# Kernel optimization log

Hardware: AMD Instinct MI355X
Metric: run time of the kernel (lower is better)

## Reference

```python
import jax, jax.numpy as jnp
import numpy as np

B, N, D = 4, 2048, 1024
H, A, Lv = 8, 128, 128   # heads, attention_dim (qk), linear_dim (v)
NUM_BLOCKS = 4
QKV_W = (2 * Lv + 2 * A) * H  # 4096
NEG = -1e9


def setup_inputs() -> dict:
    key = jax.random.key(0)
    ks = jax.random.split(key, 10)
    past_lengths = jax.random.randint(ks[0], (B,), 0, N)
    past_ids = jax.random.randint(ks[1], (B, N), 0, 10000)
    past_embeddings = jax.random.normal(ks[2], (B, N, D), dtype=jnp.float32)
    # per-block parameters, stacked on leading block axis (xavier-ish scale)
    qkv_w = jax.random.normal(ks[3], (NUM_BLOCKS, D, QKV_W), dtype=jnp.float32) * (1.0 / np.sqrt(D))
    qkv_b = jnp.zeros((NUM_BLOCKS, QKV_W), dtype=jnp.float32)
    out_w = jax.random.normal(ks[4], (NUM_BLOCKS, Lv * H, D), dtype=jnp.float32) * (1.0 / np.sqrt(Lv * H))
    out_b = jnp.zeros((NUM_BLOCKS, D), dtype=jnp.float32)
    ln_g = jnp.ones((NUM_BLOCKS, D), dtype=jnp.float32)
    ln_b = jnp.zeros((NUM_BLOCKS, D), dtype=jnp.float32)
    return {"past_lengths": past_lengths, "past_ids": past_ids,
            "past_embeddings": past_embeddings, "qkv_w": qkv_w, "qkv_b": qkv_b,
            "out_w": out_w, "out_b": out_b, "ln_g": ln_g, "ln_b": ln_b}


def _layer_norm(x, g, b, eps=1e-5):
    mu = jnp.mean(x, axis=-1, keepdims=True)
    var = jnp.mean(jnp.square(x - mu), axis=-1, keepdims=True)
    return (x - mu) * jax.lax.rsqrt(var + eps) * g + b


def _block(x, mask, qw, qb, ow, ob, g, b):
    xn = _layer_norm(x, g, b)
    qkv = (xn @ qw + qb).reshape(B, N, H, 2 * Lv + 2 * A)
    q = qkv[..., :A]              # [B,N,H,A]
    k = qkv[..., A:2 * A]         # [B,N,H,A]
    v = qkv[..., 2 * A:2 * A + Lv]  # [B,N,H,Lv]
    scores = jnp.einsum('bnha,bmha->bhnm', q, k) / np.sqrt(A)
    # original: masked_fill(-inf) -> silu -> /N -> softmax; we mask after the
    # silu transform with a large-negative logit so masked weights are ~0
    logits = jnp.where(mask[:, None, :, :], jax.nn.silu(scores) / N, NEG)
    w = jax.nn.softmax(logits, axis=-1)
    attn = jnp.einsum('bhnm,bmhl->bnhl', w, v).reshape(B, N, H * Lv)
    return x + attn @ ow + ob


def reference(past_lengths, past_ids, past_embeddings, qkv_w, qkv_b, out_w, out_b, ln_g, ln_b):
    valid = past_ids != 0                                   # [B,N]
    causal = jnp.triu(jnp.ones((N, N), dtype=bool), k=1)     # faithful to buffer (triu, diag=1)
    mask = causal[None] & valid[:, None, :] & valid[:, :, None]  # [B,N,N]
    x = past_embeddings
    for i in range(NUM_BLOCKS):
        x = _block(x, mask, qkv_w[i], qkv_b[i], out_w[i], out_b[i], ln_g[i], ln_b[i])
    return x
```

## Files before the change

### kernel.cpp

```cpp
#include <hip/hip_runtime.h>

typedef __bf16 bf16_t;
typedef __bf16 bf16x8 __attribute__((ext_vector_type(8)));
typedef __bf16 bf16x4 __attribute__((ext_vector_type(4)));
typedef float f32x4 __attribute__((ext_vector_type(4)));

#define B_ 4
#define N_ 2048
#define D_ 1024
#define H_ 8
#define NB_ 4
#define M_ (B_*N_)
#define QN_ 3072
#define QKN_ 2048

__device__ __forceinline__ void async_copy16(const void* gsrc, void* ldst) {
    __builtin_amdgcn_global_load_lds(
        (const __attribute__((address_space(1))) void*)gsrc,
        (__attribute__((address_space(3))) void*)ldst, 16, 0, 0);
}

static constexpr size_t WT_OFF  = 0;
static constexpr size_t WT_SZ   = (size_t)NB_*QN_*D_*2;
static constexpr size_t OWT_OFF = WT_OFF + WT_SZ;
static constexpr size_t OWT_SZ  = (size_t)NB_*D_*D_*2;
static constexpr size_t XN_OFF  = OWT_OFF + OWT_SZ;
static constexpr size_t XN_SZ   = (size_t)M_*D_*2;
static constexpr size_t QK_OFF  = XN_OFF + XN_SZ;
static constexpr size_t QK_SZ   = (size_t)M_*QKN_*2;
static constexpr size_t VT_OFF  = QK_OFF + QK_SZ;
static constexpr size_t VT_SZ   = (size_t)32*128*N_*2;
static constexpr size_t ATT_OFF = VT_OFF + VT_SZ;
static constexpr size_t ATT_SZ  = (size_t)M_*D_*2;
static constexpr size_t QBR_OFF = ATT_OFF + ATT_SZ;
static constexpr size_t QBR_SZ  = (size_t)NB_*QN_*4;
static constexpr size_t VS_OFF  = QBR_OFF + QBR_SZ;

__global__ __launch_bounds__(256) void repack_qkvw(const float* __restrict__ qw, bf16_t* __restrict__ wt)
{
    __shared__ float tile[64][65];
    const int nb = blockIdx.z;
    const int j0 = blockIdx.x * 64, d0 = blockIdx.y * 64;
    const int tx = threadIdx.x, ty = threadIdx.y;
    const float* src = qw + (size_t)nb * D_ * 4096;
    const int jj = j0 + tx;
    const int sel = jj >> 10, rr = jj & 1023, hh = rr >> 7, aa = rr & 127;
    const int orig = hh * 512 + sel * 128 + aa;
#pragma unroll
    for (int it = 0; it < 16; ++it) {
        int dr = it * 4 + ty;
        tile[dr][tx] = src[(size_t)(d0 + dr) * 4096 + orig];
    }
    __syncthreads();
    bf16_t* dst = wt + (size_t)nb * QN_ * D_;
#pragma unroll
    for (int it = 0; it < 16; ++it) {
        int jr = it * 4 + ty;
        dst[(size_t)(j0 + jr) * D_ + d0 + tx] = (bf16_t)tile[tx][jr];
    }
}

__global__ __launch_bounds__(256) void repack_outw(const float* __restrict__ ow, bf16_t* __restrict__ owt)
{
    __shared__ float tile[64][65];
    const int nb = blockIdx.z;
    const int j0 = blockIdx.x * 64, d0 = blockIdx.y * 64;
    const int tx = threadIdx.x, ty = threadIdx.y;
    const float* src = ow + (size_t)nb * D_ * D_;
#pragma unroll
    for (int it = 0; it < 16; ++it) {
        int dr = it * 4 + ty;
        tile[dr][tx] = src[(size_t)(d0 + dr) * D_ + j0 + tx];
    }
    __syncthreads();
    bf16_t* dst = owt + (size_t)nb * D_ * D_;
#pragma unroll
    for (int it = 0; it < 16; ++it) {
        int jr = it * 4 + ty;
        dst[(size_t)(j0 + jr) * D_ + d0 + tx] = (bf16_t)tile[tx][jr];
    }
}

__global__ __launch_bounds__(256) void repack_qb(const float* __restrict__ qb, float* __restrict__ qbr)
{
    int idx = blockIdx.x * 256 + threadIdx.x;
    int nb = idx / QN_, jj = idx % QN_;
    int sel = jj >> 10, rr = jj & 1023, hh = rr >> 7, aa = rr & 127;
    qbr[idx] = qb[nb * 4096 + hh * 512 + sel * 128 + aa];
}

__global__ __launch_bounds__(256) void ln_kernel(const float* __restrict__ x, const float* __restrict__ g,
                                                 const float* __restrict__ bb, bf16_t* __restrict__ xn)
{
    const int row = blockIdx.x, tid = threadIdx.x;
    const float4 v = ((const float4*)(x + (size_t)row * D_))[tid];
    float s = v.x + v.y + v.z + v.w;
    float q = v.x * v.x + v.y * v.y + v.z * v.z + v.w * v.w;
#pragma unroll
    for (int d = 32; d >= 1; d >>= 1) { s += __shfl_xor(s, d); q += __shfl_xor(q, d); }
    __shared__ float ls[4], lq[4];
    if ((tid & 63) == 0) { ls[tid >> 6] = s; lq[tid >> 6] = q; }
    __syncthreads();
    s = ls[0] + ls[1] + ls[2] + ls[3];
    q = lq[0] + lq[1] + lq[2] + lq[3];
    const float mean = s * (1.f / 1024.f);
    const float var  = q * (1.f / 1024.f) - mean * mean;
    const float inv  = rsqrtf(var + 1e-5f);
    const float4 gg = ((const float4*)g)[tid];
    const float4 bv = ((const float4*)bb)[tid];
    bf16x4 o;
    o[0] = (bf16_t)((v.x - mean) * inv * gg.x + bv.x);
    o[1] = (bf16_t)((v.y - mean) * inv * gg.y + bv.y);
    o[2] = (bf16_t)((v.z - mean) * inv * gg.z + bv.z);
    o[3] = (bf16_t)((v.w - mean) * inv * gg.w + bv.w);
    *(bf16x4*)(xn + (size_t)row * D_ + tid * 4) = o;
}

template<bool RESID>
__global__ __launch_bounds__(256) void gemm_nt(const bf16_t* __restrict__ Am, const bf16_t* __restrict__ Bt,
                                               const float* __restrict__ bias, float* __restrict__ resid_out,
                                               bf16_t* __restrict__ outH, bf16_t* __restrict__ vtOut,
                                               int Kn, int Nn, int vSplit)
{
    __shared__ bf16_t As[128 * 32];
    __shared__ bf16_t Bs[128 * 32];
    const int tid = threadIdx.x;
    const int lane = tid & 63, wave = tid >> 6;
    const int quad = lane >> 4, l15 = lane & 15;
    const int swz = quad ^ ((l15 >> 1) & 3);
    const int slane8 = ((lane & 3) ^ ((lane >> 3) & 3)) * 8;
    const int m0 = blockIdx.y * 128, n0 = blockIdx.x * 128;
    const int mw = (wave >> 1) * 64, nw = (wave & 1) * 64;
    const int ch0 = wave * 2, ch1 = ch0 + 1;
    const int lrow = lane >> 2;
    const bf16_t* ga0 = Am + (size_t)(m0 + ch0 * 16 + lrow) * Kn + slane8;
    const bf16_t* ga1 = Am + (size_t)(m0 + ch1 * 16 + lrow) * Kn + slane8;
    const bf16_t* gb0 = Bt + (size_t)(n0 + ch0 * 16 + lrow) * Kn + slane8;
    const bf16_t* gb1 = Bt + (size_t)(n0 + ch1 * 16 + lrow) * Kn + slane8;
    bf16_t* la0 = &As[ch0 * 512]; bf16_t* la1 = &As[ch1 * 512];
    bf16_t* lb0 = &Bs[ch0 * 512]; bf16_t* lb1 = &Bs[ch1 * 512];
    f32x4 acc[4][4] = {};
    for (int kb = 0; kb < Kn; kb += 32) {
        async_copy16(ga0, la0); async_copy16(ga1, la1);
        async_copy16(gb0, lb0); async_copy16(gb1, lb1);
        ga0 += 32; ga1 += 32; gb0 += 32; gb1 += 32;
        __syncthreads();
        bf16x8 af[4], bfv[4];
#pragma unroll
        for (int i = 0; i < 4; i++) af[i] = *(const bf16x8*)(&As[(mw + i * 16 + l15) * 32 + swz * 8]);
#pragma unroll
        for (int j = 0; j < 4; j++) bfv[j] = *(const bf16x8*)(&Bs[(nw + j * 16 + l15) * 32 + swz * 8]);
#pragma unroll
        for (int i = 0; i < 4; i++)
#pragma unroll
            for (int j = 0; j < 4; j++)
                acc[i][j] = __builtin_amdgcn_mfma_f32_16x16x32_bf16(af[i], bfv[j], acc[i][j], 0, 0, 0);
        __syncthreads();
    }
    if (!RESID && n0 >= vSplit) {
#pragma unroll
        for (int i = 0; i < 4; i++) {
            const int rowg = m0 + mw + i * 16 + quad * 4;
            const int bb2 = rowg >> 11, mloc = rowg & 2047;
#pragma unroll
            for (int j = 0; j < 4; j++) {
                const int colg = n0 + nw + j * 16 + l15;
                const int hh = (colg - 2048) >> 7, ll = (colg - 2048) & 127;
                const float bv = bias[colg];
                bf16x4 sv;
#pragma unroll
                for (int r = 0; r < 4; r++) sv[r] = (bf16_t)(acc[i][j][r] + bv);
                *(bf16x4*)(vtOut + ((size_t)(bb2 * 8 + hh) * 128 + ll) * (size_t)N_ + mloc) = sv;
            }
        }
        return;
    }
#pragma unroll
    for (int i = 0; i < 4; i++) {
#pragma unroll
        for (int j = 0; j < 4; j++) {
            const int colg = n0 + nw + j * 16 + l15;
            const float bv = bias[colg];
#pragma unroll
            for (int r = 0; r < 4; r++) {
                const int rowg = m0 + mw + i * 16 + quad * 4 + r;
                const size_t off = (size_t)rowg * Nn + colg;
                const float v = acc[i][j][r] + bv;
                if (RESID) resid_out[off] += v;
                else       outH[off] = (bf16_t)v;
            }
        }
    }
}

__global__ __launch_bounds__(256) void vsum_kernel(const bf16_t* __restrict__ vt, float* __restrict__ vs)
{
    const int gid = blockIdx.x * 4 + (threadIdx.x >> 6);
    const int lane = threadIdx.x & 63;
    const bf16_t* p = vt + (size_t)gid * N_ + lane * 8;
    float s = 0.f;
#pragma unroll
    for (int c = 0; c < 4; ++c) {
        bf16x8 v = *(const bf16x8*)(p + c * 512);
#pragma unroll
        for (int u = 0; u < 8; ++u) s += (float)v[u];
    }
#pragma unroll
    for (int d = 32; d >= 1; d >>= 1) s += __shfl_xor(s, d);
    if (lane == 0) vs[gid] = s;
}

template<bool CAUSAL>
__device__ __forceinline__ void attn_tile(
    int m0, int n0, int b, int h,
    const bf16_t* __restrict__ qk, const bf16_t* __restrict__ vtb,
    const int* __restrict__ past_ids,
    bf16_t* Ks, float* vmf, bf16_t* Ps,
    const bf16x8* qf, bf16x8 onesf, float vnf,
    f32x4* oacc, f32x4& dacc)
{
    const int tid = threadIdx.x, lane = tid & 63, wave = tid >> 6;
    const int quad = lane >> 4, l15 = lane & 15;
    const int swz = quad ^ ((l15 >> 1) & 3);
    const int slane8 = ((lane & 3) ^ ((lane >> 3) & 3)) * 8;
    const int lrow = lane >> 2;
    const size_t baseq = (size_t)b * N_ * QKN_;
    const float scaleA = 0.08838834764831845f;
    const float invN = 1.f / 2048.f;

    __syncthreads();
#pragma unroll
    for (int s = 0; s < 8; ++s) {
        const int kkc = s & 3, rg = (s >> 2) + wave * 2;
        async_copy16(qk + baseq + (size_t)(m0 + rg * 16 + lrow) * QKN_ + 1024 + h * 128 + kkc * 32 + slane8,
                     &Ks[kkc * 4096 + rg * 512 + lane * 8]);
    }
    if (tid < 128) vmf[tid] = past_ids[b * N_ + m0 + tid] != 0 ? 1.f : 0.f;
    __syncthreads();

    f32x4 sacc[8] = {};
#pragma unroll
    for (int kk = 0; kk < 4; ++kk) {
#pragma unroll
        for (int j = 0; j < 8; ++j) {
            bf16x8 kf = *(const bf16x8*)&Ks[kk * 4096 + (j * 16 + l15) * 32 + swz * 8];
            sacc[j] = __builtin_amdgcn_mfma_f32_16x16x32_bf16(kf, qf[kk], sacc[j], 0, 0, 0);
        }
    }
    __syncthreads();

#pragma unroll
    for (int s = 0; s < 8; ++s) {
        const int kkc = s & 3, rg = (s >> 2) + wave * 2;
        async_copy16(vtb + (size_t)(rg * 16 + lrow) * N_ + m0 + kkc * 32 + slane8,
                     &Ks[kkc * 4096 + rg * 512 + lane * 8]);
    }

    const int dbase = CAUSAL ? (m0 - n0 - wave * 16 - l15 + quad * 4) : 0;
#pragma unroll
    for (int j = 0; j < 8; ++j) {
        f32x4 mmv = *(const f32x4*)&vmf[j * 16 + quad * 4];
        bf16x4 pv;
#pragma unroll
        for (int r = 0; r < 4; ++r) {
            const float sv = sacc[j][r] * scaleA;
            const float xc = fminf(fmaxf(sv, -4.f), 4.f);
            float sig = __builtin_fmaf(xc, 0.25f, 0.5f);
            sig = __builtin_fmaf(-(xc * 0.03125f), fabsf(xc), sig);
            float e = __builtin_fmaf(sv * sig, invN, 1.f);
            e *= mmv[r] * vnf;
            if (CAUSAL) e = (dbase + j * 16 + r > 0) ? e : 0.f;
            pv[r] = (bf16_t)e;
        }
        const int cc = (j & 1) * 2 + (quad >> 1);
        const int cp = cc ^ ((l15 >> 1) & 3);
        *(bf16x4*)&Ps[wave * 2048 + (j >> 1) * 512 + l15 * 32 + cp * 8 + (quad & 1) * 4] = pv;
    }
    __syncthreads();

#pragma unroll
    for (int kk = 0; kk < 4; ++kk) {
        bf16x8 pf = *(const bf16x8*)&Ps[wave * 2048 + kk * 512 + l15 * 32 + swz * 8];
        dacc = __builtin_amdgcn_mfma_f32_16x16x32_bf16(pf, onesf, dacc, 0, 0, 0);
#pragma unroll
        for (int j = 0; j < 8; ++j) {
            bf16x8 vf = *(const bf16x8*)&Ks[kk * 4096 + (j * 16 + l15) * 32 + swz * 8];
            oacc[j] = __builtin_amdgcn_mfma_f32_16x16x32_bf16(pf, vf, oacc[j], 0, 0, 0);
        }
    }
}

__global__ __launch_bounds__(256, 3) void attn_kernel(const bf16_t* __restrict__ qk, const bf16_t* __restrict__ vt,
                                                      const int* __restrict__ past_ids, const float* __restrict__ vsum,
                                                      bf16_t* __restrict__ att)
{
    __shared__ bf16_t Ks[4 * 128 * 32];
    __shared__ bf16_t Ps[4 * 2048];
    __shared__ float vmf[128];

    const int bx = blockIdx.x;
    const int bh = bx & 31, t = bx >> 5;
    const int b = bh >> 3, h = bh & 7;
    const int n0 = t << 6;
    const int tid = threadIdx.x, lane = tid & 63, wave = tid >> 6;
    const int quad = lane >> 4, l15 = lane & 15;
    const bf16_t* vtb = vt + (size_t)bh * 128 * N_;
    const float invN = 1.f / 2048.f;

    bf16x8 qf[4];
    {
        const bf16_t* gq = qk + (size_t)b * N_ * QKN_ + (size_t)(n0 + wave * 16 + l15) * QKN_ + h * 128 + quad * 8;
#pragma unroll
        for (int kk = 0; kk < 4; ++kk) qf[kk] = *(const bf16x8*)(gq + kk * 32);
    }
    const float vnf = past_ids[b * N_ + n0 + wave * 16 + l15] != 0 ? 1.f : 0.f;
    bf16x8 onesf;
#pragma unroll
    for (int i = 0; i < 8; ++i) onesf[i] = (bf16_t)1.f;

    f32x4 oacc[8] = {};
    f32x4 dacc = {};

    const int mt0 = t >> 1;
    attn_tile<true>(mt0 << 7, n0, b, h, qk, vtb, past_ids, Ks, vmf, Ps, qf, onesf, vnf, oacc, dacc);
    for (int mt = mt0 + 1; mt < 16; ++mt)
        attn_tile<false>(mt << 7, n0, b, h, qk, vtb, past_ids, Ks, vmf, Ps, qf, onesf, vnf, oacc, dacc);

    float vsr[8];
#pragma unroll
    for (int j = 0; j < 8; ++j) vsr[j] = vsum[bh * 128 + j * 16 + l15];
#pragma unroll
    for (int r = 0; r < 4; ++r) {
        const float dn = dacc[r];
        const bool uni = !(dn > 0.f);
        const float rc = uni ? 0.f : __builtin_amdgcn_rcpf(dn);
        const int gn = n0 + wave * 16 + quad * 4 + r;
#pragma unroll
        for (int j = 0; j < 8; ++j) {
            const int col = j * 16 + l15;
            const float ov = uni ? (vsr[j] * invN) : (oacc[j][r] * rc);
            att[(size_t)(b * N_ + gn) * 1024 + h * 128 + col] = (bf16_t)ov;
        }
    }
}

extern "C" void kernel_launch(void* const* d_in, const int* in_sizes, int n_in,
                              void* d_out, int out_size, void* d_ws, size_t ws_size,
                              hipStream_t stream) {
    (void)in_sizes; (void)n_in; (void)out_size; (void)ws_size;
    const int*   past_ids = (const int*)d_in[1];
    const float* past_emb = (const float*)d_in[2];
    const float* qkv_w    = (const float*)d_in[3];
    const float* qkv_b    = (const float*)d_in[4];
    const float* out_w    = (const float*)d_in[5];
    const float* out_b    = (const float*)d_in[6];
    const float* ln_g     = (const float*)d_in[7];
    const float* ln_b     = (const float*)d_in[8];

    float* x = (float*)d_out;
    char* ws = (char*)d_ws;
    bf16_t* WT  = (bf16_t*)(ws + WT_OFF);
    bf16_t* OWT = (bf16_t*)(ws + OWT_OFF);
    bf16_t* XN  = (bf16_t*)(ws + XN_OFF);
    bf16_t* QK  = (bf16_t*)(ws + QK_OFF);
    bf16_t* VT  = (bf16_t*)(ws + VT_OFF);
    bf16_t* ATT = (bf16_t*)(ws + ATT_OFF);
    float*  QBR = (float*)(ws + QBR_OFF);
    float*  VS  = (float*)(ws + VS_OFF);

    hipMemcpyAsync(x, past_emb, (size_t)M_ * D_ * sizeof(float), hipMemcpyDeviceToDevice, stream);
    repack_qkvw<<<dim3(48, 16, NB_), dim3(64, 4), 0, stream>>>(qkv_w, WT);
    repack_outw<<<dim3(16, 16, NB_), dim3(64, 4), 0, stream>>>(out_w, OWT);
    repack_qb<<<48, 256, 0, stream>>>(qkv_b, QBR);

    for (int layer = 0; layer < NB_; ++layer) {
        ln_kernel<<<M_, 256, 0, stream>>>(x, ln_g + layer * D_, ln_b + layer * D_, XN);
        gemm_nt<false><<<dim3(QN_ / 128, M_ / 128), 256, 0, stream>>>(
            XN, WT + (size_t)layer * QN_ * D_, QBR + layer * QN_, nullptr, QK, VT, D_, QKN_, 2048);
        vsum_kernel<<<1024, 256, 0, stream>>>(VT, VS);
        attn_kernel<<<1024, 256, 0, stream>>>(QK, VT, past_ids, VS, ATT);
        gemm_nt<true><<<dim3(D_ / 128, M_ / 128), 256, 0, stream>>>(
            ATT, OWT + (size_t)layer * D_ * D_, out_b + layer * D_, x, nullptr, nullptr, D_, D_, 1 << 30);
    }
}
```

Before: 980.8 us.

## Replace GEMM with 256x128 tiled, 4-stage async-LDS pipelined 512-thread kernel

Replaces the single-buffered 128x128 GEMM with a 256x128 tile computed by 8 waves. Global-to-LDS copies go through a 4-slot ring buffer with 3 stages prefetched ahead, using explicit vmcnt waits and raw barriers in place of __syncthreads. MFMA sections are also bracketed with s_setprio. This is meant to hide global load latency behind MFMA work and raise reuse per block. In exchange it uses 96KB of LDS and runs fewer blocks, and the hand-tuned waitcnt logic could race if the counts are wrong.

Measured after the change: 929.5 us. 1.06x faster.

```diff
diff --git a/kernel.cpp b/kernel.cpp
--- a/kernel.cpp
+++ b/kernel.cpp
@@ -117,73 +117,99 @@
 }
 
 template<bool RESID>
-__global__ __launch_bounds__(256) void gemm_nt(const bf16_t* __restrict__ Am, const bf16_t* __restrict__ Bt,
-                                               const float* __restrict__ bias, float* __restrict__ resid_out,
-                                               bf16_t* __restrict__ outH, bf16_t* __restrict__ vtOut,
-                                               int Kn, int Nn, int vSplit)
-{
-    __shared__ bf16_t As[128 * 32];
-    __shared__ bf16_t Bs[128 * 32];
+__global__ __launch_bounds__(512, 2) void gemm256(const bf16_t* __restrict__ Am, const bf16_t* __restrict__ Bt,
+                                                  const float* __restrict__ bias, float* __restrict__ resid_out,
+                                                  bf16_t* __restrict__ outH, bf16_t* __restrict__ vtOut,
+                                                  int Kn, int Nn, int vSplit)
+{
+    __shared__ bf16_t As[4 * 256 * 32];
+    __shared__ bf16_t Bs[4 * 128 * 32];
     const int tid = threadIdx.x;
     const int lane = tid & 63, wave = tid >> 6;
+    const int wr = wave >> 2, wc = wave & 3;
     const int quad = lane >> 4, l15 = lane & 15;
     const int swz = quad ^ ((l15 >> 1) & 3);
     const int slane8 = ((lane & 3) ^ ((lane >> 3) & 3)) * 8;
-    const int m0 = blockIdx.y * 128, n0 = blockIdx.x * 128;
-    const int mw = (wave >> 1) * 64, nw = (wave & 1) * 64;
-    const int ch0 = wave * 2, ch1 = ch0 + 1;
     const int lrow = lane >> 2;
-    const bf16_t* ga0 = Am + (size_t)(m0 + ch0 * 16 + lrow) * Kn + slane8;
-    const bf16_t* ga1 = Am + (size_t)(m0 + ch1 * 16 + lrow) * Kn + slane8;
-    const bf16_t* gb0 = Bt + (size_t)(n0 + ch0 * 16 + lrow) * Kn + slane8;
-    const bf16_t* gb1 = Bt + (size_t)(n0 + ch1 * 16 + lrow) * Kn + slane8;
-    bf16_t* la0 = &As[ch0 * 512]; bf16_t* la1 = &As[ch1 * 512];
-    bf16_t* lb0 = &Bs[ch0 * 512]; bf16_t* lb1 = &Bs[ch1 * 512];
-    f32x4 acc[4][4] = {};
-    for (int kb = 0; kb < Kn; kb += 32) {
-        async_copy16(ga0, la0); async_copy16(ga1, la1);
-        async_copy16(gb0, lb0); async_copy16(gb1, lb1);
-        ga0 += 32; ga1 += 32; gb0 += 32; gb1 += 32;
-        __syncthreads();
-        bf16x8 af[4], bfv[4];
-#pragma unroll
-        for (int i = 0; i < 4; i++) af[i] = *(const bf16x8*)(&As[(mw + i * 16 + l15) * 32 + swz * 8]);
-#pragma unroll
-        for (int j = 0; j < 4; j++) bfv[j] = *(const bf16x8*)(&Bs[(nw + j * 16 + l15) * 32 + swz * 8]);
-#pragma unroll
-        for (int i = 0; i < 4; i++)
-#pragma unroll
-            for (int j = 0; j < 4; j++)
+    const int m0 = blockIdx.y * 256, n0 = blockIdx.x * 128;
+
+    const int chA0 = wave * 2, chA1 = chA0 + 1;
+    const bf16_t* gA0 = Am + (size_t)(m0 + chA0 * 16 + lrow) * Kn + slane8;
+    const bf16_t* gA1 = Am + (size_t)(m0 + chA1 * 16 + lrow) * Kn + slane8;
+    const bf16_t* gB  = Bt + (size_t)(n0 + wave * 16 + lrow) * Kn + slane8;
+    bf16_t* const dA0 = &As[chA0 * 512];
+    bf16_t* const dA1 = &As[chA1 * 512];
+    bf16_t* const dB  = &Bs[wave * 512];
+
+    auto STAGE = [&](int slot) {
+        async_copy16(gA0, dA0 + slot * 8192);
+        async_copy16(gA1, dA1 + slot * 8192);
+        async_copy16(gB,  dB  + slot * 4096);
+        gA0 += 32; gA1 += 32; gB += 32;
+    };
+
+    f32x4 acc[8][2] = {};
+    const int NT = Kn >> 5;
+
+    STAGE(0); STAGE(1); STAGE(2);
+    asm volatile("s_waitcnt vmcnt(6)" ::: "memory");
+    __builtin_amdgcn_s_barrier();
+
+    const int aoff = (wr * 128 + l15) * 32 + swz * 8;
+    const int boff = (wc * 32  + l15) * 32 + swz * 8;
+
+    for (int t = 0; t < NT; ++t) {
+        const int ring = t & 3;
+        const bf16_t* ra = &As[ring * 8192 + aoff];
+        const bf16_t* rb = &Bs[ring * 4096 + boff];
+        bf16x8 af[8], bfv[2];
+#pragma unroll
+        for (int i = 0; i < 8; ++i) af[i] = *(const bf16x8*)(ra + i * 512);
+#pragma unroll
+        for (int j = 0; j < 2; ++j) bfv[j] = *(const bf16x8*)(rb + j * 512);
+        if (t + 3 < NT) STAGE((t + 3) & 3);
+        __builtin_amdgcn_s_barrier();
+        asm volatile("s_waitcnt lgkmcnt(0)" ::: "memory");
+        __builtin_amdgcn_s_setprio(1);
+#pragma unroll
+        for (int i = 0; i < 8; ++i)
+#pragma unroll
+            for (int j = 0; j < 2; ++j)
                 acc[i][j] = __builtin_amdgcn_mfma_f32_16x16x32_bf16(af[i], bfv[j], acc[i][j], 0, 0, 0);
-        __syncthreads();
-    }
+        __builtin_amdgcn_s_setprio(0);
+        if (t + 3 < NT)      asm volatile("s_waitcnt vmcnt(6)" ::: "memory");
+        else if (t + 2 < NT) asm volatile("s_waitcnt vmcnt(3)" ::: "memory");
+        else if (t + 1 < NT) asm volatile("s_waitcnt vmcnt(0)" ::: "memory");
+        __builtin_amdgcn_s_barrier();
+    }
+
     if (!RESID && n0 >= vSplit) {
 #pragma unroll
-        for (int i = 0; i < 4; i++) {
-            const int rowg = m0 + mw + i * 16 + quad * 4;
+        for (int i = 0; i < 8; ++i) {
+            const int rowg = m0 + wr * 128 + i * 16 + quad * 4;
             const int bb2 = rowg >> 11, mloc = rowg & 2047;
 #pragma unroll
-            for (int j = 0; j < 4; j++) {
-                const int colg = n0 + nw + j * 16 + l15;
+            for (int j = 0; j < 2; ++j) {
+                const int colg = n0 + wc * 32 + j * 16 + l15;
                 const int hh = (colg - 2048) >> 7, ll = (colg - 2048) & 127;
                 const float bv = bias[colg];
                 bf16x4 sv;
 #pragma unroll
-                for (int r = 0; r < 4; r++) sv[r] = (bf16_t)(acc[i][j][r] + bv);
+                for (int r = 0; r < 4; ++r) sv[r] = (bf16_t)(acc[i][j][r] + bv);
                 *(bf16x4*)(vtOut + ((size_t)(bb2 * 8 + hh) * 128 + ll) * (size_t)N_ + mloc) = sv;
             }
         }
         return;
     }
 #pragma unroll
-    for (int i = 0; i < 4; i++) {
-#pragma unroll
-        for (int j = 0; j < 4; j++) {
-            const int colg = n0 + nw + j * 16 + l15;
+    for (int i = 0; i < 8; ++i) {
+#pragma unroll
+        for (int j = 0; j < 2; ++j) {
+            const int colg = n0 + wc * 32 + j * 16 + l15;
             const float bv = bias[colg];
 #pragma unroll
-            for (int r = 0; r < 4; r++) {
-                const int rowg = m0 + mw + i * 16 + quad * 4 + r;
+            for (int r = 0; r < 4; ++r) {
+                const int rowg = m0 + wr * 128 + i * 16 + quad * 4 + r;
                 const size_t off = (size_t)rowg * Nn + colg;
                 const float v = acc[i][j][r] + bv;
                 if (RESID) resid_out[off] += v;
@@ -375,11 +401,11 @@
 
     for (int layer = 0; layer < NB_; ++layer) {
         ln_kernel<<<M_, 256, 0, stream>>>(x, ln_g + layer * D_, ln_b + layer * D_, XN);
-        gemm_nt<false><<<dim3(QN_ / 128, M_ / 128), 256, 0, stream>>>(
+        gemm256<false><<<dim3(QN_ / 128, M_ / 256), 512, 0, stream>>>(
             XN, WT + (size_t)layer * QN_ * D_, QBR + layer * QN_, nullptr, QK, VT, D_, QKN_, 2048);
         vsum_kernel<<<1024, 256, 0, stream>>>(VT, VS);
         attn_kernel<<<1024, 256, 0, stream>>>(QK, VT, past_ids, VS, ATT);
-        gemm_nt<true><<<dim3(D_ / 128, M_ / 128), 256, 0, stream>>>(
+        gemm256<true><<<dim3(D_ / 128, M_ / 256), 512, 0, stream>>>(
             ATT, OWT + (size_t)layer * D_ * D_, out_b + layer * D_, x, nullptr, nullptr, D_, D_, 1 << 30);
     }
 }
```
